# Performance work log

Hardware: AMD Instinct MI355X
Metric: run time of the kernel (lower is better)

Reference implementation:

```python
import jax, jax.numpy as jnp
import numpy as np

B = 1                 # images
GRID = 30             # patch grid per side (HEIGHT_FACTOR*2)
NIMG = GRID * GRID    # 900 tokens per image
EMBED = 1152
HEADS = 16
DH = EMBED // HEADS   # 72
DHH = DH // 2         # 36
LAYERS = 6
FF = 4608             # mlp intermediate (4*EMBED)
MERGE = 2
MHID = EMBED * MERGE * MERGE   # 4608 merger hidden
OUT = 2048
DS_IDX = (2, 5)
PS = 16               # spatial patch size
TP = 2                # temporal patch size
THETA = 10000.0


def _rope_cos_sin():
    # 2D rotary positions in merge-block order: (Hf, Wf, mh, mw)
    HF = GRID // MERGE
    I, J, MH, MW = np.meshgrid(np.arange(HF), np.arange(HF), np.arange(MERGE), np.arange(MERGE), indexing='ij')
    hpos = (I * MERGE + MH).reshape(-1).astype(np.float32)
    wpos = (J * MERGE + MW).reshape(-1).astype(np.float32)
    inv = 1.0 / (THETA ** (np.arange(0, DHH, 2, dtype=np.float32) / DHH))      # [DH//4]
    rot = np.concatenate([hpos[:, None] * inv, wpos[:, None] * inv], axis=-1)  # [NIMG, DHH]
    cos = np.concatenate([np.cos(rot), np.cos(rot)], axis=-1)[None, None]      # [1,1,NIMG,DH]
    sin = np.concatenate([np.sin(rot), np.sin(rot)], axis=-1)[None, None]
    return jnp.asarray(cos, jnp.float32), jnp.asarray(sin, jnp.float32)


def _ln(x, w, b, eps=1e-6):
    mu = x.mean(-1, keepdims=True)
    xc = x - mu
    v = (xc * xc).mean(-1, keepdims=True)
    return xc * jax.lax.rsqrt(v + eps) * w + b


def _rot_half(t):
    t1, t2 = jnp.split(t, 2, axis=-1)
    return jnp.concatenate([-t2, t1], axis=-1)


def setup_inputs():
    key = jax.random.key(0)
    ks = jax.random.split(key, 12)
    s = 0.02
    n = lambda k, sh: jax.random.normal(k, sh, jnp.float32) * s
    z = lambda sh: jnp.zeros(sh, jnp.float32)
    o = lambda sh: jnp.ones(sh, jnp.float32)
    cos, sin = _rope_cos_sin()
    return {
        'pixel_values': jax.random.uniform(ks[0], (B, 1, 3, GRID * PS, GRID * PS), jnp.float32) * 255.0,
        'patch_w': n(ks[1], (EMBED, 3 * TP * PS * PS)), 'patch_b': z((EMBED,)),
        'pos_emb': n(ks[2], (1, NIMG, EMBED)),
        'cos': cos, 'sin': sin,
        'ln1_w': o((LAYERS, EMBED)), 'ln1_b': z((LAYERS, EMBED)),
        'qkv_w': n(ks[3], (LAYERS, 3 * EMBED, EMBED)), 'qkv_b': z((LAYERS, 3 * EMBED)),
        'proj_w': n(ks[4], (LAYERS, EMBED, EMBED)), 'proj_b': z((LAYERS, EMBED)),
        'ln2_w': o((LAYERS, EMBED)), 'ln2_b': z((LAYERS, EMBED)),
        'fc1_w': n(ks[5], (LAYERS, FF, EMBED)), 'fc1_b': z((LAYERS, FF)),
        'fc2_w': n(ks[6], (LAYERS, EMBED, FF)), 'fc2_b': z((LAYERS, EMBED)),
        'ds_norm_w': o((2, MHID)), 'ds_norm_b': z((2, MHID)),
        'ds_fc1_w': n(ks[7], (2, MHID, MHID)), 'ds_fc1_b': z((2, MHID)),
        'ds_fc2_w': n(ks[8], (2, OUT, MHID)), 'ds_fc2_b': z((2, OUT)),
        'm_norm_w': o((EMBED,)), 'm_norm_b': z((EMBED,)),
        'm_fc1_w': n(ks[9], (MHID, MHID)), 'm_fc1_b': z((MHID,)),
        'm_fc2_w': n(ks[10], (OUT, MHID)), 'm_fc2_b': z((OUT,)),
    }


def _forward(pixel_values, patch_w, patch_b, pos_emb, cos, sin, ln1_w, ln1_b, qkv_w, qkv_b, proj_w, proj_b, ln2_w, ln2_b, fc1_w, fc1_b, fc2_w, fc2_b, ds_norm_w, ds_norm_b, ds_fc1_w, ds_fc1_b, ds_fc2_w, ds_fc2_b, m_norm_w, m_norm_b, m_fc1_w, m_fc1_b, m_fc2_w, m_fc2_b):
    HF = GRID // MERGE
    x = (pixel_values - 127.5) * (1.0 / 127.5)                 # [B,1,3,H,W]
    x = jnp.concatenate([x, x], axis=1)                        # temporal duplication -> [B,2,3,H,W]
    x = x.reshape(B, 1, TP, 3, HF, MERGE, PS, HF, MERGE, PS)
    x = jnp.transpose(x, (0, 1, 4, 7, 5, 8, 3, 2, 6, 9))       # [B,1,HF,WF,mh,mw,3,TP,ps,ps]
    x = x.reshape(-1, 3 * TP * PS * PS)                        # [B*NIMG, 1536] (conv3d == matmul)
    h = (x @ patch_w.T + patch_b).reshape(1, -1, EMBED)        # [1, N, E]
    N = B * NIMG
    h = h + jnp.tile(pos_emb, (1, B, 1))
    cosf = jnp.tile(cos, (1, 1, B, 1))                         # [1,1,N,DH]
    sinf = jnp.tile(sin, (1, 1, B, 1))
    ds = []
    for l in range(LAYERS):
        hn = _ln(h, ln1_w[l], ln1_b[l])
        qkv = (hn @ qkv_w[l].T + qkv_b[l]).reshape(N, 3, HEADS, DH)
        qkv = jnp.transpose(qkv, (1, 2, 0, 3))                 # [3, H, N, dh]
        q, k, v = qkv[0][None], qkv[1][None], qkv[2][None]     # [1, H, N, dh]
        q = q * cosf + _rot_half(q) * sinf                     # inline RoPE (q,k pre-scaled by dh**-0.25 in weights)
        k = k * cosf + _rot_half(k) * sinf
        qb = jnp.transpose(q[0].reshape(HEADS, B, NIMG, DH), (1, 0, 2, 3))  # per-image attention blocks
        kb = jnp.transpose(k[0].reshape(HEADS, B, NIMG, DH), (1, 0, 2, 3))
        vb = jnp.transpose(v[0].reshape(HEADS, B, NIMG, DH), (1, 0, 2, 3))
        attn = jax.nn.softmax(jnp.einsum('bhqd,bhkd->bhqk', qb, kb), axis=-1)
        o = jnp.einsum('bhqk,bhkd->bhqd', attn, vb)            # [B, H, NIMG, dh]
        o = jnp.transpose(o, (0, 2, 1, 3)).reshape(1, N, EMBED)
        h = h + (o @ proj_w[l].T + proj_b[l])
        m = jax.nn.gelu(_ln(h, ln2_w[l], ln2_b[l]) @ fc1_w[l].T + fc1_b[l], approximate=True)
        h = h + (m @ fc2_w[l].T + fc2_b[l])
        if l in DS_IDX:
            d = DS_IDX.index(l)
            xm = _ln(h.reshape(1, -1, MHID), ds_norm_w[d], ds_norm_b[d])
            xm = jax.nn.gelu(xm @ ds_fc1_w[d].T + ds_fc1_b[d], approximate=True) @ ds_fc2_w[d].T + ds_fc2_b[d]
            ds.append(xm)                                      # [1, N/4, OUT]
    hm = _ln(h, m_norm_w, m_norm_b).reshape(1, -1, MHID)
    out = jax.nn.gelu(hm @ m_fc1_w.T + m_fc1_b, approximate=True) @ m_fc2_w.T + m_fc2_b
    return ds, out


def reference(pixel_values, patch_w, patch_b, pos_emb, cos, sin, ln1_w, ln1_b, qkv_w, qkv_b, proj_w, proj_b, ln2_w, ln2_b, fc1_w, fc1_b, fc2_w, fc2_b, ds_norm_w, ds_norm_b, ds_fc1_w, ds_fc1_b, ds_fc2_w, ds_fc2_b, m_norm_w, m_norm_b, m_fc1_w, m_fc1_b, m_fc2_w, m_fc2_b):
    ds, out = _forward(pixel_values, patch_w, patch_b, pos_emb, cos, sin, ln1_w, ln1_b, qkv_w, qkv_b, proj_w, proj_b, ln2_w, ln2_b, fc1_w, fc1_b, fc2_w, fc2_b, ds_norm_w, ds_norm_b, ds_fc1_w, ds_fc1_b, ds_fc2_w, ds_fc2_b, m_norm_w, m_norm_b, m_fc1_w, m_fc1_b, m_fc2_w, m_fc2_b)
    return (*ds, out)
```

## Files before the change

### kernel.cpp

```cpp
#include <hip/hip_runtime.h>
#include <hip/hip_bf16.h>
#include <cstdint>

#define NT   900
#define EMB  1152
#define NH   16
#define DHD  72
#define DHH  36
#define DHP  96
#define KVP  928
#define NL   6
#define FFD  4608
#define MHD  4608
#define OUTD 2048
#define NM   225

typedef __attribute__((ext_vector_type(8))) short short8;
typedef __attribute__((ext_vector_type(4))) float f32x4;

__device__ __forceinline__ ushort f2bf(float f) {
    uint32_t u = __float_as_uint(f);
    uint32_t r = u + 0x7FFF + ((u >> 16) & 1);
    return (ushort)(r >> 16);
}
__device__ __forceinline__ float gelu_f(float x) {
    return 0.5f * x * (1.0f + tanhf(0.7978845608f * (x + 0.044715f * x * x * x)));
}

__device__ __forceinline__ void g2lds16(const ushort* g, ushort* l) {
    __builtin_amdgcn_global_load_lds(
        (const __attribute__((address_space(1))) unsigned int*)g,
        (__attribute__((address_space(3))) unsigned int*)l, 16, 0, 0);
}

__global__ __launch_bounds__(256) void k_cvt(const float* __restrict__ src,
                                             ushort* __restrict__ dst, int n4) {
    int idx = blockIdx.x * 256 + threadIdx.x;
    if (idx >= n4) return;
    const float4 v = *(const float4*)(src + (size_t)idx * 4);
    ushort o[4] = { f2bf(v.x), f2bf(v.y), f2bf(v.z), f2bf(v.w) };
    *(uint2*)(dst + (size_t)idx * 4) = *(const uint2*)o;
}

__global__ __launch_bounds__(256) void k_patch(const float* __restrict__ pix,
                                               ushort* __restrict__ xp) {
    int idx = blockIdx.x * 256 + threadIdx.x;
    if (idx >= NT * 1536) return;
    int t = idx / 1536, f = idx - t * 1536;
    int mw = t & 1, mh = (t >> 1) & 1;
    int tq = t >> 2;
    int jj = tq % 15, ii = tq / 15;
    int pw = f & 15, ph = (f >> 4) & 15, c = f >> 9;
    int Hi = (ii * 2 + mh) * 16 + ph;
    int Wi = (jj * 2 + mw) * 16 + pw;
    float p = pix[((size_t)c * 480 + Hi) * 480 + Wi];
    xp[idx] = f2bf((p - 127.5f) * (1.0f / 127.5f));
}

__global__ __launch_bounds__(256) void k_ln(const float* __restrict__ x,
                                            const float* __restrict__ w,
                                            const float* __restrict__ b,
                                            ushort* __restrict__ y, int C) {
    int row = blockIdx.x;
    int tid = threadIdx.x;
    const float* xr = x + (size_t)row * C;
    float s = 0.f, ss = 0.f;
    for (int c = tid; c < C; c += 256) { float v = xr[c]; s += v; ss += v * v; }
    for (int off = 32; off; off >>= 1) {
        s  += __shfl_down(s,  off, 64);
        ss += __shfl_down(ss, off, 64);
    }
    __shared__ float rs[4], rss[4];
    int wid = tid >> 6, lane = tid & 63;
    if (lane == 0) { rs[wid] = s; rss[wid] = ss; }
    __syncthreads();
    float S  = rs[0] + rs[1] + rs[2] + rs[3];
    float SS = rss[0] + rss[1] + rss[2] + rss[3];
    float mu  = S / C;
    float var = SS / C - mu * mu;
    float inv = rsqrtf(var + 1e-6f);
    ushort* yr = y + (size_t)row * C;
    for (int c = tid; c < C; c += 256) yr[c] = f2bf((xr[c] - mu) * inv * w[c] + b[c]);
}

__global__ __launch_bounds__(256) void k_fixln(const float* __restrict__ part,
                                               const float* __restrict__ bias,
                                               const float* __restrict__ res,
                                               float* __restrict__ hout,
                                               const float* __restrict__ lw,
                                               const float* __restrict__ lb,
                                               ushort* __restrict__ y,
                                               int C, int S, long MN) {
    int row = blockIdx.x, tid = threadIdx.x;
    int C4 = C >> 2;
    const float* prow = part + (size_t)row * C;
    const float* rrow = res + (size_t)row * C;
    float* hrow = hout + (size_t)row * C;
    ushort* yrow = y + (size_t)row * C;

    float4 vals[2];
    float s = 0.f, ss = 0.f;
    int idx[2] = { tid, tid + 256 };
#pragma unroll
    for (int it = 0; it < 2; ++it) {
        int c4 = idx[it];
        if (c4 < C4) {
            float4 v = *(const float4*)(prow + c4 * 4);
            for (int sI = 1; sI < S; ++sI) {
                const float4 p = *(const float4*)(prow + (size_t)sI * MN + c4 * 4);
                v.x += p.x; v.y += p.y; v.z += p.z; v.w += p.w;
            }
            const float4 bi = *(const float4*)(bias + c4 * 4);
            v.x += bi.x; v.y += bi.y; v.z += bi.z; v.w += bi.w;
            const float4 rr = *(const float4*)(rrow + c4 * 4);
            v.x += rr.x; v.y += rr.y; v.z += rr.z; v.w += rr.w;
            *(float4*)(hrow + c4 * 4) = v;
            vals[it] = v;
            s  += v.x + v.y + v.z + v.w;
            ss += v.x * v.x + v.y * v.y + v.z * v.z + v.w * v.w;
        }
    }
    for (int off = 32; off; off >>= 1) {
        s  += __shfl_down(s,  off, 64);
        ss += __shfl_down(ss, off, 64);
    }
    __shared__ float rs[4], rss[4];
    int wid = tid >> 6, lane = tid & 63;
    if (lane == 0) { rs[wid] = s; rss[wid] = ss; }
    __syncthreads();
    float St  = rs[0] + rs[1] + rs[2] + rs[3];
    float SSt = rss[0] + rss[1] + rss[2] + rss[3];
    float mu  = St / C;
    float var = SSt / C - mu * mu;
    float inv = rsqrtf(var + 1e-6f);
#pragma unroll
    for (int it = 0; it < 2; ++it) {
        int c4 = idx[it];
        if (c4 < C4) {
            float4 v = vals[it];
            const float4 w4 = *(const float4*)(lw + c4 * 4);
            const float4 b4 = *(const float4*)(lb + c4 * 4);
            ushort o[4] = { f2bf((v.x - mu) * inv * w4.x + b4.x),
                            f2bf((v.y - mu) * inv * w4.y + b4.y),
                            f2bf((v.z - mu) * inv * w4.z + b4.z),
                            f2bf((v.w - mu) * inv * w4.w + b4.w) };
            *(uint2*)(yrow + c4 * 4) = *(const uint2*)o;
        }
    }
}

template <int ACT, int OBF16, int SPLIT>
__global__ __launch_bounds__(256) void k_bgs(const ushort* __restrict__ A,
                                             const ushort* __restrict__ W,
                                             const float* __restrict__ bias,
                                             const float* __restrict__ res,
                                             void* __restrict__ Cp,
                                             float* __restrict__ part,
                                             int M, int N, int K, int S) {
    __shared__ __align__(16) ushort As[64 * 64];
    __shared__ __align__(16) ushort Bs[64 * 64];
    int tid = threadIdx.x;

    int nwg  = gridDim.x * gridDim.y * gridDim.z;
    int orig = blockIdx.x + gridDim.x * (blockIdx.y + gridDim.y * blockIdx.z);
    int xcd = orig & 7, loc = orig >> 3;
    int q8 = nwg >> 3, r8 = nwg & 7;
    int work = (xcd < r8 ? xcd * (q8 + 1) : r8 * (q8 + 1) + (xcd - r8) * q8) + loc;
    int bx = work % gridDim.x;
    int rest = work / gridDim.x;
    int by = rest % gridDim.y;
    int bz = rest / gridDim.y;

    int row0 = bx * 64, col0 = by * 64;
    int z = bz;
    int Kc = K / S;
    int kbeg = z * Kc;
    int steps = Kc >> 6;

    int w = tid >> 6, lane = tid & 63;
    int lrow = lane >> 3;
    int cg   = ((lane & 7) ^ lrow) << 3;

    int ar0 = row0 + w * 16 + lrow; if (ar0 > M - 1) ar0 = M - 1;
    int ar1 = row0 + w * 16 + 8 + lrow; if (ar1 > M - 1) ar1 = M - 1;
    int wr0 = col0 + w * 16 + lrow;
    int wr1 = wr0 + 8;
    const ushort* ap0 = A + (size_t)ar0 * K + kbeg + cg;
    const ushort* ap1 = A + (size_t)ar1 * K + kbeg + cg;
    const ushort* wp0 = W + (size_t)wr0 * K + kbeg + cg;
    const ushort* wp1 = W + (size_t)wr1 * K + kbeg + cg;
    ushort* asd0 = &As[(w * 16) * 64];
    ushort* asd1 = &As[(w * 16 + 8) * 64];
    ushort* bsd0 = &Bs[(w * 16) * 64];
    ushort* bsd1 = &Bs[(w * 16 + 8) * 64];

    int fr = lane & 15, kg8 = (lane >> 4) << 3;
    int wrr = (w >> 1) * 32, wcc = (w & 1) * 32;
    int sw = (fr & 7) << 3;

    f32x4 acc[2][2] = {};
    for (int s = 0; s < steps; ++s) {
        int kk = s << 6;
        __syncthreads();
        g2lds16(ap0 + kk, asd0);
        g2lds16(ap1 + kk, asd1);
        g2lds16(wp0 + kk, bsd0);
        g2lds16(wp1 + kk, bsd1);
        __syncthreads();
#pragma unroll
        for (int j = 0; j < 2; ++j) {
            int ko = j * 32 + kg8;
            int kx = ko ^ sw;
            short8 a0 = *(const short8*)&As[(wrr + fr) * 64 + kx];
            short8 a1 = *(const short8*)&As[(wrr + 16 + fr) * 64 + kx];
            short8 b0 = *(const short8*)&Bs[(wcc + fr) * 64 + kx];
            short8 b1 = *(const short8*)&Bs[(wcc + 16 + fr) * 64 + kx];
            acc[0][0] = __builtin_amdgcn_mfma_f32_16x16x32_bf16(a0, b0, acc[0][0], 0, 0, 0);
            acc[0][1] = __builtin_amdgcn_mfma_f32_16x16x32_bf16(a0, b1, acc[0][1], 0, 0, 0);
            acc[1][0] = __builtin_amdgcn_mfma_f32_16x16x32_bf16(a1, b0, acc[1][0], 0, 0, 0);
            acc[1][1] = __builtin_amdgcn_mfma_f32_16x16x32_bf16(a1, b1, acc[1][1], 0, 0, 0);
        }
    }

#pragma unroll
    for (int fi = 0; fi < 2; fi++)
#pragma unroll
        for (int fj = 0; fj < 2; fj++)
#pragma unroll
            for (int r = 0; r < 4; r++) {
                int row = row0 + wrr + fi * 16 + (lane >> 4) * 4 + r;
                int col = col0 + wcc + fj * 16 + fr;
                if (row < M) {
                    if (SPLIT) {
                        part[((size_t)z * M + row) * N + col] = acc[fi][fj][r];
                    } else {
                        float v = acc[fi][fj][r] + bias[col];
                        if (res) v += res[(size_t)row * N + col];
                        if (ACT == 1) v = gelu_f(v);
                        if (OBF16) ((ushort*)Cp)[(size_t)row * N + col] = f2bf(v);
                        else       ((float*)Cp)[(size_t)row * N + col] = v;
                    }
                }
            }
}

template <int ACT, int OBF16>
__global__ __launch_bounds__(256) void k_fix(const float* __restrict__ part,
                                             const float* __restrict__ bias,
                                             const float* __restrict__ res,
                                             void* __restrict__ Cp,
                                             int M, int N, int S) {
    size_t idx = (size_t)blockIdx.x * 256 + threadIdx.x;
    size_t total = (size_t)M * N / 4;
    if (idx >= total) return;
    size_t e = idx * 4;
    int row = (int)(e / N), col = (int)(e - (size_t)row * N);
    float4 v = *(const float4*)(part + e);
    for (int s = 1; s < S; ++s) {
        const float4 p = *(const float4*)(part + (size_t)s * M * N + e);
        v.x += p.x; v.y += p.y; v.z += p.z; v.w += p.w;
    }
    const float4 bi = *(const float4*)(bias + col);
    v.x += bi.x; v.y += bi.y; v.z += bi.z; v.w += bi.w;
    if (res) {
        const float4 rr = *(const float4*)(res + e);
        v.x += rr.x; v.y += rr.y; v.z += rr.z; v.w += rr.w;
    }
    if (ACT == 1) { v.x = gelu_f(v.x); v.y = gelu_f(v.y); v.z = gelu_f(v.z); v.w = gelu_f(v.w); }
    if (OBF16) {
        ushort o[4] = { f2bf(v.x), f2bf(v.y), f2bf(v.z), f2bf(v.w) };
        *(uint2*)((ushort*)Cp + e) = *(const uint2*)o;
    } else {
        *(float4*)((float*)Cp + e) = v;
    }
}

template <int OBF16>
__global__ __launch_bounds__(256) void k_mm(const ushort* __restrict__ A,
                                            const ushort* __restrict__ Wb,
                                            void* __restrict__ Cp,
                                            int M, int N, int K, int ldc, int Nw,
                                            long as_, long ws_, long cs_) {
    __shared__ __align__(16) ushort As[64 * 40];
    __shared__ __align__(16) ushort Bs[64 * 40];
    int z = blockIdx.z;
    A  += (size_t)z * as_;
    Wb += (size_t)z * ws_;
    float*  Cf = (float*)Cp + (size_t)z * cs_;
    ushort* Cb = (ushort*)Cp + (size_t)z * cs_;

    int tid = threadIdx.x;
    int row0 = blockIdx.y * 64, col0 = blockIdx.x * 64;

    int sm = tid >> 2, sp = tid & 3;
    int ar = row0 + sm; if (ar > M - 1) ar = M - 1;
    int wr = col0 + sm; if (wr > N - 1) wr = N - 1;
    const ushort* aptr = A + (size_t)ar * K;

    int lane = tid & 63, wid = tid >> 6;
    int wrr = (wid >> 1) * 32, wcc = (wid & 1) * 32;
    int fr = lane & 15, kg = lane >> 4;

    f32x4 acc[2][2] = {};

    for (int k0 = 0; k0 < K; k0 += 32) {
        *(uint4*)&As[sm * 40 + sp * 8] = *(const uint4*)(aptr + k0 + sp * 8);
        *(uint4*)&Bs[sm * 40 + sp * 8] = *(const uint4*)(Wb + (size_t)wr * K + k0 + sp * 8);
        __syncthreads();
        short8 a0 = *(const short8*)&As[(wrr + fr) * 40 + kg * 8];
        short8 a1 = *(const short8*)&As[(wrr + 16 + fr) * 40 + kg * 8];
        short8 b0 = *(const short8*)&Bs[(wcc + fr) * 40 + kg * 8];
        short8 b1 = *(const short8*)&Bs[(wcc + 16 + fr) * 40 + kg * 8];
        acc[0][0] = __builtin_amdgcn_mfma_f32_16x16x32_bf16(a0, b0, acc[0][0], 0, 0, 0);
        acc[0][1] = __builtin_amdgcn_mfma_f32_16x16x32_bf16(a0, b1, acc[0][1], 0, 0, 0);
        acc[1][0] = __builtin_amdgcn_mfma_f32_16x16x32_bf16(a1, b0, acc[1][0], 0, 0, 0);
        acc[1][1] = __builtin_amdgcn_mfma_f32_16x16x32_bf16(a1, b1, acc[1][1], 0, 0, 0);
        __syncthreads();
    }

#pragma unroll
    for (int fi = 0; fi < 2; fi++)
#pragma unroll
        for (int fj = 0; fj < 2; fj++)
#pragma unroll
            for (int r = 0; r < 4; r++) {
                int row = row0 + wrr + fi * 16 + (lane >> 4) * 4 + r;
                int col = col0 + wcc + fj * 16 + (lane & 15);
                if (row < M && col < Nw) {
                    float v = acc[fi][fj][r];
                    if (OBF16) Cb[(size_t)row * ldc + col] = f2bf(v);
                    else       Cf[(size_t)row * ldc + col] = v;
                }
            }
}

__global__ __launch_bounds__(256) void k_rope(const float* __restrict__ qkv,
                                              const float* __restrict__ cs,
                                              const float* __restrict__ sn,
                                              ushort* __restrict__ q,
                                              ushort* __restrict__ k,
                                              ushort* __restrict__ vt) {
    int idx = blockIdx.x * 256 + threadIdx.x;
    if (idx >= NT * NH * DHP) return;
    int t = idx / (NH * DHP);
    int rem = idx - t * (NH * DHP);
    int h = rem / DHP, d = rem - h * DHP;
    size_t oi = ((size_t)h * NT + t) * DHP + d;
    if (d < DHD) {
        const float* base = qkv + (size_t)t * 3 * EMB;
        float c = cs[t * DHD + d], s = sn[t * DHD + d];
        int   d2 = (d < DHH) ? d + DHH : d - DHH;
        float sg = (d < DHH) ? -1.f : 1.f;
        int e = h * DHD + d;
        float qv = base[e] * c + sg * base[h * DHD + d2] * s;
        float kv = base[EMB + e] * c + sg * base[EMB + h * DHD + d2] * s;
        q[oi] = f2bf(qv);
        k[oi] = f2bf(kv);
        vt[((size_t)h * DHP + d) * KVP + t] = f2bf(base[2 * EMB + e]);
    } else {
        q[oi] = 0;
        k[oi] = 0;
    }
}

__global__ __launch_bounds__(256) void k_vpad(ushort* __restrict__ vt) {
    int idx = blockIdx.x * 256 + threadIdx.x;
    int tot = NH * DHP * (KVP - NT);
    if (idx >= tot) return;
    int pw = KVP - NT;
    int hd = idx / pw, j = idx - hd * pw;
    vt[(size_t)hd * KVP + NT + j] = 0;
}

__global__ __launch_bounds__(256) void k_sm(const float* __restrict__ S,
                                            ushort* __restrict__ P) {
    int row = blockIdx.x * 4 + (threadIdx.x >> 6);
    int lane = threadIdx.x & 63;
    const float* sp = S + (size_t)row * KVP;
    ushort* pp = P + (size_t)row * KVP;
    float v[15];
#pragma unroll
    for (int i = 0; i < 15; i++) {
        int kt = lane + i * 64;
        v[i] = (kt < NT) ? sp[kt] : -1e30f;
    }
    float mx = -1e30f;
#pragma unroll
    for (int i = 0; i < 15; i++) mx = fmaxf(mx, v[i]);
    for (int off = 32; off; off >>= 1) mx = fmaxf(mx, __shfl_xor(mx, off, 64));
    float sum = 0.f;
#pragma unroll
    for (int i = 0; i < 15; i++) {
        int kt = lane + i * 64;
        v[i] = (kt < NT) ? __expf(v[i] - mx) : 0.f;
        sum += v[i];
    }
    for (int off = 32; off; off >>= 1) sum += __shfl_xor(sum, off, 64);
    float inv = 1.f / sum;
#pragma unroll
    for (int i = 0; i < 15; i++) {
        int kt = lane + i * 64;
        if (kt < KVP) pp[kt] = f2bf(v[i] * inv);
    }
}

extern "C" void kernel_launch(void* const* d_in, const int* in_sizes, int n_in,
                              void* d_out, int out_size, void* d_ws, size_t ws_size,
                              hipStream_t stream) {
    const float* pix     = (const float*)d_in[0];
    const float* patch_w = (const float*)d_in[1];
    const float* patch_b = (const float*)d_in[2];
    const float* pos_emb = (const float*)d_in[3];
    const float* cosb    = (const float*)d_in[4];
    const float* sinb    = (const float*)d_in[5];
    const float* ln1_w   = (const float*)d_in[6];
    const float* ln1_b   = (const float*)d_in[7];
    const float* qkv_w   = (const float*)d_in[8];
    const float* qkv_b   = (const float*)d_in[9];
    const float* proj_w  = (const float*)d_in[10];
    const float* proj_b  = (const float*)d_in[11];
    const float* ln2_w   = (const float*)d_in[12];
    const float* ln2_b   = (const float*)d_in[13];
    const float* fc1_w   = (const float*)d_in[14];
    const float* fc1_b   = (const float*)d_in[15];
    const float* fc2_w   = (const float*)d_in[16];
    const float* fc2_b   = (const float*)d_in[17];
    const float* dsn_w   = (const float*)d_in[18];
    const float* dsn_b   = (const float*)d_in[19];
    const float* ds1_w   = (const float*)d_in[20];
    const float* ds1_b   = (const float*)d_in[21];
    const float* ds2_w   = (const float*)d_in[22];
    const float* ds2_b   = (const float*)d_in[23];
    const float* mn_w    = (const float*)d_in[24];
    const float* mn_b    = (const float*)d_in[25];
    const float* mf1_w   = (const float*)d_in[26];
    const float* mf1_b   = (const float*)d_in[27];
    const float* mf2_w   = (const float*)d_in[28];
    const float* mf2_b   = (const float*)d_in[29];
    float* out = (float*)d_out;

    float* wsf = (float*)d_ws;
    size_t off = 0;
    auto af = [&](size_t n) { float* p = wsf + off; off += (n + 3) & ~(size_t)3; return p; };
    float* h    = af((size_t)NT * EMB);
    float* qkv  = af((size_t)NT * 3 * EMB);
    float* part = af((size_t)4 * NT * EMB);
    float* S    = af((size_t)NH * NT * KVP);
    ushort* wsh = (ushort*)(wsf + off);
    size_t hoff = 0;
    auto ah = [&](size_t n) { ushort* p = wsh + hoff; hoff += (n + 7) & ~(size_t)7; return p; };
    ushort* hn  = ah((size_t)NT * EMB);
    ushort* hn2 = ah((size_t)NM * MHD);
    ushort* qb  = ah((size_t)NH * NT * DHP);
    ushort* kb  = ah((size_t)NH * NT * DHP);
    ushort* vt  = ah((size_t)NH * DHP * KVP);
    ushort* P   = ah((size_t)NH * NT * KVP);
    ushort* ob  = ah((size_t)NT * EMB);
    ushort* t1  = ah((size_t)NT * FFD);
    ushort* xp  = t1;
    ushort* w_patch = ah((size_t)EMB * 1536);
    ushort* w_qkv   = ah((size_t)NL * 3 * EMB * EMB);
    ushort* w_proj  = ah((size_t)NL * EMB * EMB);
    ushort* w_fc1   = ah((size_t)NL * FFD * EMB);
    ushort* w_fc2   = ah((size_t)NL * EMB * FFD);
    ushort* w_ds1   = ah((size_t)2 * MHD * MHD);
    ushort* w_ds2   = ah((size_t)2 * OUTD * MHD);
    ushort* w_mf1   = ah((size_t)MHD * MHD);
    ushort* w_mf2   = ah((size_t)OUTD * MHD);

    const long QS = (long)NT * DHP;
    const long VS = (long)DHP * KVP;
    const long SS = (long)NT * KVP;
    const long MN = (long)NT * EMB;

    const int MB  = (NT + 63) / 64;
    const int MBm = (NM + 63) / 64;
    auto fixg = [](int M, int N) { return dim3(((size_t)M * N / 4 + 255) / 256); };
    auto cvt = [&](const float* s, ushort* d, size_t n) {
        k_cvt<<<dim3((unsigned)((n / 4 + 255) / 256)), 256, 0, stream>>>(s, d, (int)(n / 4));
    };

    cvt(patch_w, w_patch, (size_t)EMB * 1536);
    cvt(qkv_w,   w_qkv,   (size_t)NL * 3 * EMB * EMB);
    cvt(proj_w,  w_proj,  (size_t)NL * EMB * EMB);
    cvt(fc1_w,   w_fc1,   (size_t)NL * FFD * EMB);
    cvt(fc2_w,   w_fc2,   (size_t)NL * EMB * FFD);
    cvt(ds1_w,   w_ds1,   (size_t)2 * MHD * MHD);
    cvt(ds2_w,   w_ds2,   (size_t)2 * OUTD * MHD);
    cvt(mf1_w,   w_mf1,   (size_t)MHD * MHD);
    cvt(mf2_w,   w_mf2,   (size_t)OUTD * MHD);

    k_patch<<<dim3((NT * 1536 + 255) / 256), 256, 0, stream>>>(pix, xp);
    k_vpad<<<dim3((NH * DHP * (KVP - NT) + 255) / 256), 256, 0, stream>>>(vt);
    k_bgs<0, 0, 1><<<dim3(MB, EMB / 64, 2), 256, 0, stream>>>(
        xp, w_patch, nullptr, nullptr, nullptr, part, NT, EMB, 1536, 2);
    k_fixln<<<NT, 256, 0, stream>>>(part, patch_b, pos_emb, h,
                                    ln1_w, ln1_b, hn, EMB, 2, MN);

    for (int l = 0; l < NL; ++l) {
        k_bgs<0, 0, 0><<<dim3(MB, 3 * EMB / 64, 1), 256, 0, stream>>>(
            hn, w_qkv + (size_t)l * 3 * EMB * EMB, qkv_b + l * 3 * EMB, nullptr, qkv,
            nullptr, NT, 3 * EMB, EMB, 1);
        k_rope<<<dim3((NT * NH * DHP + 255) / 256), 256, 0, stream>>>(
            qkv, cosb, sinb, qb, kb, vt);
        k_mm<0><<<dim3(MB, MB, NH), 256, 0, stream>>>(
            qb, kb, S, NT, NT, DHP, KVP, NT, QS, QS, SS);
        k_sm<<<dim3(NH * NT / 4), 256, 0, stream>>>(S, P);
        k_mm<1><<<dim3(2, MB, NH), 256, 0, stream>>>(
            P, vt, ob, NT, DHD, KVP, EMB, DHD, SS, VS, DHD);
        k_bgs<0, 0, 1><<<dim3(MB, EMB / 64, 3), 256, 0, stream>>>(
            ob, w_proj + (size_t)l * EMB * EMB, nullptr, nullptr, nullptr, part,
            NT, EMB, EMB, 3);
        k_fixln<<<NT, 256, 0, stream>>>(part, proj_b + l * EMB, h, h,
                                        ln2_w + l * EMB, ln2_b + l * EMB, hn,
                                        EMB, 3, MN);
        k_bgs<1, 1, 0><<<dim3(MB, FFD / 64, 1), 256, 0, stream>>>(
            hn, w_fc1 + (size_t)l * FFD * EMB, fc1_b + l * FFD, nullptr, t1,
            nullptr, NT, FFD, EMB, 1);
        const float* nlw = (l == NL - 1) ? mn_w : ln1_w + (l + 1) * EMB;
        const float* nlb = (l == NL - 1) ? mn_b : ln1_b + (l + 1) * EMB;
        k_bgs<0, 0, 1><<<dim3(MB, EMB / 64, 4), 256, 0, stream>>>(
            t1, w_fc2 + (size_t)l * EMB * FFD, nullptr, nullptr, nullptr, part,
            NT, EMB, FFD, 4);
        k_fixln<<<NT, 256, 0, stream>>>(part, fc2_b + l * EMB, h, h,
                                        nlw, nlb, hn, EMB, 4, MN);
        if (l == 2 || l == 5) {
            int d = (l == 2) ? 0 : 1;
            k_ln<<<NM, 256, 0, stream>>>(h, dsn_w + d * MHD, dsn_b + d * MHD, hn2, MHD);
            k_bgs<0, 0, 1><<<dim3(MBm, MHD / 64, 4), 256, 0, stream>>>(
                hn2, w_ds1 + (size_t)d * MHD * MHD, nullptr, nullptr, nullptr, part,
                NM, MHD, MHD, 4);
            k_fix<1, 1><<<fixg(NM, MHD), 256, 0, stream>>>(part, ds1_b + d * MHD,
                                                           nullptr, t1, NM, MHD, 4);
            k_bgs<0, 0, 1><<<dim3(MBm, OUTD / 64, 4), 256, 0, stream>>>(
                t1, w_ds2 + (size_t)d * OUTD * MHD, nullptr, nullptr, nullptr, part,
                NM, OUTD, MHD, 4);
            k_fix<0, 0><<<fixg(NM, OUTD), 256, 0, stream>>>(
                part, ds2_b + d * OUTD, nullptr, out + (size_t)d * NM * OUTD,
                NM, OUTD, 4);
        }
    }
    k_bgs<0, 0, 1><<<dim3(MBm, MHD / 64, 4), 256, 0, stream>>>(
        hn, w_mf1, nullptr, nullptr, nullptr, part, NM, MHD, MHD, 4);
    k_fix<1, 1><<<fixg(NM, MHD), 256, 0, stream>>>(part, mf1_b, nullptr, t1, NM, MHD, 4);
    k_bgs<0, 0, 1><<<dim3(MBm, OUTD / 64, 4), 256, 0, stream>>>(
        t1, w_mf2, nullptr, nullptr, nullptr, part, NM, OUTD, MHD, 4);
    k_fix<0, 0><<<fixg(NM, OUTD), 256, 0, stream>>>(
        part, mf2_b, nullptr, out + (size_t)2 * NM * OUTD, NM, OUTD, 4);
}
```

Before: 1.380 ms.

## Use async-LDS MFMA kernel for P·V, pad buffers, batch weight conversion

Replaces the generic bf16-output matmul for attention P·V with a dedicated kernel that loads swizzled 64-wide K tiles through global_load_lds and works on P and V buffers padded to 960 columns (V to 128 rows). Softmax now writes the padded P columns without a bounds check. The nine weight-conversion launches are merged into one kernel. XCD-aware block remapping is added to the score matmul. These changes target launch overhead and inefficient loads in the attention matmuls, at the cost of extra memory for padding and a larger zero-fill of V.

```diff
diff --git a/kernel.cpp b/kernel.cpp
--- a/kernel.cpp
+++ b/kernel.cpp
@@ -9,6 +9,8 @@
 #define DHH  36
 #define DHP  96
 #define KVP  928
+#define PW   960
+#define VR   128
 #define NL   6
 #define FFD  4608
 #define MHD  4608
@@ -33,13 +35,27 @@
         (__attribute__((address_space(3))) unsigned int*)l, 16, 0, 0);
 }
 
-__global__ __launch_bounds__(256) void k_cvt(const float* __restrict__ src,
-                                             ushort* __restrict__ dst, int n4) {
-    int idx = blockIdx.x * 256 + threadIdx.x;
-    if (idx >= n4) return;
-    const float4 v = *(const float4*)(src + (size_t)idx * 4);
+__device__ __forceinline__ int xcd_remap(int orig, int nwg) {
+    int xcd = orig & 7, loc = orig >> 3;
+    int q8 = nwg >> 3, r8 = nwg & 7;
+    return (xcd < r8 ? xcd * (q8 + 1) : r8 * (q8 + 1) + (xcd - r8) * q8) + loc;
+}
+
+struct CvtArgs {
+    const float* src[9];
+    ushort* dst[9];
+    long off[10];
+};
+__global__ __launch_bounds__(256) void k_cvt9(CvtArgs a) {
+    long idx = (long)blockIdx.x * 256 + threadIdx.x;
+    if (idx >= a.off[9]) return;
+    int g = 0;
+#pragma unroll
+    for (int i = 1; i < 9; ++i) if (idx >= a.off[i]) g = i;
+    long li = idx - a.off[g];
+    const float4 v = *(const float4*)(a.src[g] + li * 4);
     ushort o[4] = { f2bf(v.x), f2bf(v.y), f2bf(v.z), f2bf(v.w) };
-    *(uint2*)(dst + (size_t)idx * 4) = *(const uint2*)o;
+    *(uint2*)(a.dst[g] + li * 4) = *(const uint2*)o;
 }
 
 __global__ __launch_bounds__(256) void k_patch(const float* __restrict__ pix,
@@ -163,9 +179,7 @@
 
     int nwg  = gridDim.x * gridDim.y * gridDim.z;
     int orig = blockIdx.x + gridDim.x * (blockIdx.y + gridDim.y * blockIdx.z);
-    int xcd = orig & 7, loc = orig >> 3;
-    int q8 = nwg >> 3, r8 = nwg & 7;
-    int work = (xcd < r8 ? xcd * (q8 + 1) : r8 * (q8 + 1) + (xcd - r8) * q8) + loc;
+    int work = xcd_remap(orig, nwg);
     int bx = work % gridDim.x;
     int rest = work / gridDim.x;
     int by = rest % gridDim.y;
@@ -244,6 +258,83 @@
             }
 }
 
+__global__ __launch_bounds__(256) void k_att(const ushort* __restrict__ P,
+                                             const ushort* __restrict__ Vt,
+                                             ushort* __restrict__ ob) {
+    __shared__ __align__(16) ushort As[64 * 64];
+    __shared__ __align__(16) ushort Bs[64 * 64];
+    int tid = threadIdx.x;
+
+    int nwg  = gridDim.x * gridDim.y * gridDim.z;
+    int orig = blockIdx.x + gridDim.x * (blockIdx.y + gridDim.y * blockIdx.z);
+    int work = xcd_remap(orig, nwg);
+    int bx = work % gridDim.x;
+    int rest = work / gridDim.x;
+    int by = rest % gridDim.y;
+    int h  = rest / gridDim.y;
+
+    int row0 = bx * 64, col0 = by * 64;
+    const ushort* Ah = P  + (size_t)h * NT * PW;
+    const ushort* Wh = Vt + (size_t)h * VR * PW;
+
+    int w = tid >> 6, lane = tid & 63;
+    int lrow = lane >> 3;
+    int cg   = ((lane & 7) ^ lrow) << 3;
+
+    int ar0 = row0 + w * 16 + lrow; if (ar0 > NT - 1) ar0 = NT - 1;
+    int ar1 = row0 + w * 16 + 8 + lrow; if (ar1 > NT - 1) ar1 = NT - 1;
+    int wr0 = col0 + w * 16 + lrow;
+    int wr1 = wr0 + 8;
+    const ushort* ap0 = Ah + (size_t)ar0 * PW + cg;
+    const ushort* ap1 = Ah + (size_t)ar1 * PW + cg;
+    const ushort* wp0 = Wh + (size_t)wr0 * PW + cg;
+    const ushort* wp1 = Wh + (size_t)wr1 * PW + cg;
+    ushort* asd0 = &As[(w * 16) * 64];
+    ushort* asd1 = &As[(w * 16 + 8) * 64];
+    ushort* bsd0 = &Bs[(w * 16) * 64];
+    ushort* bsd1 = &Bs[(w * 16 + 8) * 64];
+
+    int fr = lane & 15, kg8 = (lane >> 4) << 3;
+    int wrr = (w >> 1) * 32, wcc = (w & 1) * 32;
+    int sw = (fr & 7) << 3;
+
+    f32x4 acc[2][2] = {};
+    for (int s = 0; s < 15; ++s) {
+        int kk = s << 6;
+        __syncthreads();
+        g2lds16(ap0 + kk, asd0);
+        g2lds16(ap1 + kk, asd1);
+        g2lds16(wp0 + kk, bsd0);
+        g2lds16(wp1 + kk, bsd1);
+        __syncthreads();
+#pragma unroll
+        for (int j = 0; j < 2; ++j) {
+            int ko = j * 32 + kg8;
+            int kx = ko ^ sw;
+            short8 a0 = *(const short8*)&As[(wrr + fr) * 64 + kx];
+            short8 a1 = *(const short8*)&As[(wrr + 16 + fr) * 64 + kx];
+            short8 b0 = *(const short8*)&Bs[(wcc + fr) * 64 + kx];
+            short8 b1 = *(const short8*)&Bs[(wcc + 16 + fr) * 64 + kx];
+            acc[0][0] = __builtin_amdgcn_mfma_f32_16x16x32_bf16(a0, b0, acc[0][0], 0, 0, 0);
+            acc[0][1] = __builtin_amdgcn_mfma_f32_16x16x32_bf16(a0, b1, acc[0][1], 0, 0, 0);
+            acc[1][0] = __builtin_amdgcn_mfma_f32_16x16x32_bf16(a1, b0, acc[1][0], 0, 0, 0);
+            acc[1][1] = __builtin_amdgcn_mfma_f32_16x16x32_bf16(a1, b1, acc[1][1], 0, 0, 0);
+        }
+    }
+
+#pragma unroll
+    for (int fi = 0; fi < 2; fi++)
+#pragma unroll
+        for (int fj = 0; fj < 2; fj++)
+#pragma unroll
+            for (int r = 0; r < 4; r++) {
+                int row = row0 + wrr + fi * 16 + (lane >> 4) * 4 + r;
+                int col = col0 + wcc + fj * 16 + fr;
+                if (row < NT && col < DHD)
+                    ob[(size_t)row * EMB + h * DHD + col] = f2bf(acc[fi][fj][r]);
+            }
+}
+
 template <int ACT, int OBF16>
 __global__ __launch_bounds__(256) void k_fix(const float* __restrict__ part,
                                              const float* __restrict__ bias,
@@ -275,22 +366,27 @@
     }
 }
 
-template <int OBF16>
 __global__ __launch_bounds__(256) void k_mm(const ushort* __restrict__ A,
                                             const ushort* __restrict__ Wb,
-                                            void* __restrict__ Cp,
+                                            float* __restrict__ Cf,
                                             int M, int N, int K, int ldc, int Nw,
                                             long as_, long ws_, long cs_) {
     __shared__ __align__(16) ushort As[64 * 40];
     __shared__ __align__(16) ushort Bs[64 * 40];
-    int z = blockIdx.z;
+    int nwg  = gridDim.x * gridDim.y * gridDim.z;
+    int orig = blockIdx.x + gridDim.x * (blockIdx.y + gridDim.y * blockIdx.z);
+    int work = xcd_remap(orig, nwg);
+    int bx = work % gridDim.x;
+    int rest = work / gridDim.x;
+    int by = rest % gridDim.y;
+    int z  = rest / gridDim.y;
+
     A  += (size_t)z * as_;
     Wb += (size_t)z * ws_;
-    float*  Cf = (float*)Cp + (size_t)z * cs_;
-    ushort* Cb = (ushort*)Cp + (size_t)z * cs_;
+    Cf += (size_t)z * cs_;
 
     int tid = threadIdx.x;
-    int row0 = blockIdx.y * 64, col0 = blockIdx.x * 64;
+    int row0 = by * 64, col0 = bx * 64;
 
     int sm = tid >> 2, sp = tid & 3;
     int ar = row0 + sm; if (ar > M - 1) ar = M - 1;
@@ -326,11 +422,8 @@
             for (int r = 0; r < 4; r++) {
                 int row = row0 + wrr + fi * 16 + (lane >> 4) * 4 + r;
                 int col = col0 + wcc + fj * 16 + (lane & 15);
-                if (row < M && col < Nw) {
-                    float v = acc[fi][fj][r];
-                    if (OBF16) Cb[(size_t)row * ldc + col] = f2bf(v);
-                    else       Cf[(size_t)row * ldc + col] = v;
-                }
+                if (row < M && col < Nw)
+                    Cf[(size_t)row * ldc + col] = acc[fi][fj][r];
             }
 }
 
@@ -356,20 +449,19 @@
         float kv = base[EMB + e] * c + sg * base[EMB + h * DHD + d2] * s;
         q[oi] = f2bf(qv);
         k[oi] = f2bf(kv);
-        vt[((size_t)h * DHP + d) * KVP + t] = f2bf(base[2 * EMB + e]);
+        vt[((size_t)h * VR + d) * PW + t] = f2bf(base[2 * EMB + e]);
     } else {
         q[oi] = 0;
         k[oi] = 0;
     }
 }
 
-__global__ __launch_bounds__(256) void k_vpad(ushort* __restrict__ vt) {
+__global__ __launch_bounds__(256) void k_vzero(ushort* __restrict__ vt) {
     int idx = blockIdx.x * 256 + threadIdx.x;
-    int tot = NH * DHP * (KVP - NT);
+    int tot = NH * VR * PW / 8;
     if (idx >= tot) return;
-    int pw = KVP - NT;
-    int hd = idx / pw, j = idx - hd * pw;
-    vt[(size_t)hd * KVP + NT + j] = 0;
+    uint4 z = { 0, 0, 0, 0 };
+    *(uint4*)(vt + (size_t)idx * 8) = z;
 }
 
 __global__ __launch_bounds__(256) void k_sm(const float* __restrict__ S,
@@ -377,7 +469,7 @@
     int row = blockIdx.x * 4 + (threadIdx.x >> 6);
     int lane = threadIdx.x & 63;
     const float* sp = S + (size_t)row * KVP;
-    ushort* pp = P + (size_t)row * KVP;
+    ushort* pp = P + (size_t)row * PW;
     float v[15];
 #pragma unroll
     for (int i = 0; i < 15; i++) {
@@ -400,7 +492,7 @@
 #pragma unroll
     for (int i = 0; i < 15; i++) {
         int kt = lane + i * 64;
-        if (kt < KVP) pp[kt] = f2bf(v[i] * inv);
+        pp[kt] = f2bf(v[i] * inv);
     }
 }
 
@@ -453,8 +545,8 @@
     ushort* hn2 = ah((size_t)NM * MHD);
     ushort* qb  = ah((size_t)NH * NT * DHP);
     ushort* kb  = ah((size_t)NH * NT * DHP);
-    ushort* vt  = ah((size_t)NH * DHP * KVP);
-    ushort* P   = ah((size_t)NH * NT * KVP);
+    ushort* vt  = ah((size_t)NH * VR * PW);
+    ushort* P   = ah((size_t)NH * NT * PW);
     ushort* ob  = ah((size_t)NT * EMB);
     ushort* t1  = ah((size_t)NT * FFD);
     ushort* xp  = t1;
@@ -469,29 +561,29 @@
     ushort* w_mf2   = ah((size_t)OUTD * MHD);
 
     const long QS = (long)NT * DHP;
-    const long VS = (long)DHP * KVP;
     const long SS = (long)NT * KVP;
     const long MN = (long)NT * EMB;
 
     const int MB  = (NT + 63) / 64;
     const int MBm = (NM + 63) / 64;
     auto fixg = [](int M, int N) { return dim3(((size_t)M * N / 4 + 255) / 256); };
-    auto cvt = [&](const float* s, ushort* d, size_t n) {
-        k_cvt<<<dim3((unsigned)((n / 4 + 255) / 256)), 256, 0, stream>>>(s, d, (int)(n / 4));
-    };
-
-    cvt(patch_w, w_patch, (size_t)EMB * 1536);
-    cvt(qkv_w,   w_qkv,   (size_t)NL * 3 * EMB * EMB);
-    cvt(proj_w,  w_proj,  (size_t)NL * EMB * EMB);
-    cvt(fc1_w,   w_fc1,   (size_t)NL * FFD * EMB);
-    cvt(fc2_w,   w_fc2,   (size_t)NL * EMB * FFD);
-    cvt(ds1_w,   w_ds1,   (size_t)2 * MHD * MHD);
-    cvt(ds2_w,   w_ds2,   (size_t)2 * OUTD * MHD);
-    cvt(mf1_w,   w_mf1,   (size_t)MHD * MHD);
-    cvt(mf2_w,   w_mf2,   (size_t)OUTD * MHD);
+
+    CvtArgs ca;
+    const float* srcs[9] = { patch_w, qkv_w, proj_w, fc1_w, fc2_w, ds1_w, ds2_w, mf1_w, mf2_w };
+    ushort* dsts[9] = { w_patch, w_qkv, w_proj, w_fc1, w_fc2, w_ds1, w_ds2, w_mf1, w_mf2 };
+    long lens[9] = { (long)EMB * 1536, (long)NL * 3 * EMB * EMB, (long)NL * EMB * EMB,
+                     (long)NL * FFD * EMB, (long)NL * EMB * FFD, (long)2 * MHD * MHD,
+                     (long)2 * OUTD * MHD, (long)MHD * MHD, (long)OUTD * MHD };
+    ca.off[0] = 0;
+    for (int i = 0; i < 9; ++i) {
+        ca.src[i] = srcs[i];
+        ca.dst[i] = dsts[i];
+        ca.off[i + 1] = ca.off[i] + lens[i] / 4;
+    }
+    k_cvt9<<<dim3((unsigned)((ca.off[9] + 255) / 256)), 256, 0, stream>>>(ca);
 
     k_patch<<<dim3((NT * 1536 + 255) / 256), 256, 0, stream>>>(pix, xp);
-    k_vpad<<<dim3((NH * DHP * (KVP - NT) + 255) / 256), 256, 0, stream>>>(vt);
+    k_vzero<<<dim3((NH * VR * PW / 8 + 255) / 256), 256, 0, stream>>>(vt);
     k_bgs<0, 0, 1><<<dim3(MB, EMB / 64, 2), 256, 0, stream>>>(
         xp, w_patch, nullptr, nullptr, nullptr, part, NT, EMB, 1536, 2);
     k_fixln<<<NT, 256, 0, stream>>>(part, patch_b, pos_emb, h,
@@ -503,11 +595,10 @@
             nullptr, NT, 3 * EMB, EMB, 1);
         k_rope<<<dim3((NT * NH * DHP + 255) / 256), 256, 0, stream>>>(
             qkv, cosb, sinb, qb, kb, vt);
-        k_mm<0><<<dim3(MB, MB, NH), 256, 0, stream>>>(
+        k_mm<<<dim3(MB, MB, NH), 256, 0, stream>>>(
             qb, kb, S, NT, NT, DHP, KVP, NT, QS, QS, SS);
         k_sm<<<dim3(NH * NT / 4), 256, 0, stream>>>(S, P);
-        k_mm<1><<<dim3(2, MB, NH), 256, 0, stream>>>(
-            P, vt, ob, NT, DHD, KVP, EMB, DHD, SS, VS, DHD);
+        k_att<<<dim3(MB, 2, NH), 256, 0, stream>>>(P, vt, ob);
         k_bgs<0, 0, 1><<<dim3(MB, EMB / 64, 3), 256, 0, stream>>>(
             ob, w_proj + (size_t)l * EMB * EMB, nullptr, nullptr, nullptr, part,
             NT, EMB, EMB, 3);
```

Result: faster. 1.297 ms (-6.0%).
